# Kernel optimization log

Hardware: AMD Instinct MI355X
Metric: run time of the kernel (lower is better)

## Reference

```python
import jax, jax.numpy as jnp
import numpy as np

NQ, NT, NA = 10000, 50000, 50000
E_GR, E_LT, E_SIM, E_COMP, E_GEN = 50000, 50000, 80000, 100000, 50000
HID, NH, HC, DOT, NL = 512, 4, 128, 256, 2
NEG_SLOPE = 0.2  # PyG GATv2Conv default negative_slope


def _gatv2(x_src, x_dst, src, dst, Wl, bl, Wr, br, att, bias, n_dst):
    # GATv2: x_j = lin_l(x_src), x_i = lin_r(x_dst); e = att . leaky_relu(x_i + x_j)
    xl = (x_src @ Wl + bl).reshape(-1, NH, HC)   # [Ns,H,C]
    xr = (x_dst @ Wr + br).reshape(-1, NH, HC)   # [Nd,H,C]
    m = jax.nn.leaky_relu(xl[src] + xr[dst], NEG_SLOPE)      # [E,H,C]
    logits = jnp.einsum('ehc,hc->eh', m, att)                # [E,H]
    lmax = jax.lax.stop_gradient(jax.ops.segment_max(logits, dst, num_segments=n_dst))
    lmax = jnp.where(jnp.isfinite(lmax), lmax, 0.0)
    ex = jnp.exp(logits - lmax[dst])
    denom = jax.ops.segment_sum(ex, dst, num_segments=n_dst)
    alpha = ex / (denom[dst] + 1e-16)                        # softmax over incoming edges
    out = jax.ops.segment_sum(xl[src] * alpha[:, :, None], dst, num_segments=n_dst)
    return out.reshape(n_dst, NH * HC) + bias


def _layernorm(x, g, b):
    mu = x.mean(-1, keepdims=True)
    var = ((x - mu) ** 2).mean(-1, keepdims=True)
    return (x - mu) / jnp.sqrt(var + 1e-5) * g + b


def _forward(xq, xt, xa, answer_features,
             qp_W, qp_b, tp_W, tp_b, ap_W, ap_b,
             afp_W1, afp_b1, afp_W2, afp_b2,
             conv_Wl, conv_bl, conv_Wr, conv_br, conv_att, conv_bias,
             qh_W, qh_b, qh_g, qh_beta, rh_W, rh_b, rh_g, rh_beta, score_bias,
             ei_gr, ei_lt, ei_sim, ei_comp, ei_gen):
    hq = xq @ qp_W + qp_b
    ht = xt @ tp_W + tp_b
    ha = xa @ ap_W + ap_b
    # add_self_loops=True only for ('query','similar_to','query')
    loops = jnp.arange(NQ, dtype=ei_sim.dtype)
    sim_src = jnp.concatenate([ei_sim[0], loops])
    sim_dst = jnp.concatenate([ei_sim[1], loops])
    for l in range(NL):
        P = lambda r: (conv_Wl[l, r], conv_bl[l, r], conv_Wr[l, r], conv_br[l, r], conv_att[l, r], conv_bias[l, r])
        o_gr = _gatv2(hq, ht, ei_gr[0], ei_gr[1], *P(0), NT)          # query -> think
        o_rgr = _gatv2(ht, hq, ei_gr[1], ei_gr[0], *P(1), NQ)         # think -> query (rev)
        o_lt = _gatv2(ht, ha, ei_lt[0], ei_lt[1], *P(2), NA)          # think -> answer
        o_rlt = _gatv2(ha, ht, ei_lt[1], ei_lt[0], *P(3), NT)         # answer -> think (rev)
        o_sim = _gatv2(hq, hq, sim_src, sim_dst, *P(4), NQ)           # query -> query
        o_cmp = _gatv2(ht, ht, ei_comp[0], ei_comp[1], *P(5), NT)     # think -> think
        # HeteroConv aggr='mean' across relations per destination type, then relu
        hq = jax.nn.relu((o_rgr + o_sim) / 2.0)
        ht = jax.nn.relu((o_gr + o_rlt + o_cmp) / 3.0)
        ha = jax.nn.relu(o_lt)
    q_emb = hq[ei_gen[0]]
    a_emb = ha[ei_gen[1]]
    t_emb = ht[ei_gen[1]]  # faithful to source: think indexed with answer-side index
    af_emb = jax.nn.relu(answer_features @ afp_W1 + afp_b1) @ afp_W2 + afp_b2
    q = _layernorm(q_emb @ qh_W + qh_b, qh_g, qh_beta)
    r = _layernorm(jnp.concatenate([t_emb, a_emb, af_emb], -1) @ rh_W + rh_b, rh_g, rh_beta)
    return (q * r).sum(-1) / jnp.sqrt(jnp.float32(DOT)) + score_bias


def setup_inputs() -> dict:
    ks = jax.random.split(jax.random.key(0), 40)
    n = lambda j, shape, s=0.05: jax.random.normal(ks[j], shape, jnp.float32) * s
    ri = lambda j, shape, hi: jax.random.randint(ks[j], shape, 0, hi, jnp.int32)
    return dict(
        xq=n(0, (NQ, 384), 1.0), xt=n(1, (NT, 384), 1.0), xa=n(2, (NA, 384), 1.0),
        answer_features=n(3, (E_GEN, 6), 1.0),
        qp_W=n(4, (384, HID)), qp_b=n(5, (HID,)),
        tp_W=n(6, (384, HID)), tp_b=n(7, (HID,)),
        ap_W=n(8, (384, HID)), ap_b=n(9, (HID,)),
        afp_W1=n(10, (6, 64)), afp_b1=n(11, (64,)),
        afp_W2=n(12, (64, HID)), afp_b2=n(13, (HID,)),
        conv_Wl=n(14, (NL, 6, HID, HID)), conv_bl=n(15, (NL, 6, HID)),
        conv_Wr=n(16, (NL, 6, HID, HID)), conv_br=n(17, (NL, 6, HID)),
        conv_att=n(18, (NL, 6, NH, HC)), conv_bias=n(19, (NL, 6, HID)),
        qh_W=n(20, (HID, DOT)), qh_b=n(21, (DOT,)),
        qh_g=jnp.ones((DOT,), jnp.float32), qh_beta=jnp.zeros((DOT,), jnp.float32),
        rh_W=n(22, (HID * 3, DOT)), rh_b=n(23, (DOT,)),
        rh_g=jnp.ones((DOT,), jnp.float32), rh_beta=jnp.zeros((DOT,), jnp.float32),
        score_bias=jnp.zeros((1,), jnp.float32),
        ei_gr=jnp.stack([ri(24, (E_GR,), NQ), ri(25, (E_GR,), NT)]),
        ei_lt=jnp.stack([ri(26, (E_LT,), NT), ri(27, (E_LT,), NA)]),
        ei_sim=ri(28, (2, E_SIM), NQ),
        ei_comp=ri(29, (2, E_COMP), NT),
        ei_gen=jnp.stack([ri(30, (E_GEN,), NQ), ri(31, (E_GEN,), NA)]),
    )


def reference(xq, xt, xa, answer_features,
              qp_W, qp_b, tp_W, tp_b, ap_W, ap_b,
              afp_W1, afp_b1, afp_W2, afp_b2,
              conv_Wl, conv_bl, conv_Wr, conv_br, conv_att, conv_bias,
              qh_W, qh_b, qh_g, qh_beta, rh_W, rh_b, rh_g, rh_beta, score_bias,
              ei_gr, ei_lt, ei_sim, ei_comp, ei_gen):
    return _forward(xq, xt, xa, answer_features,
                    qp_W, qp_b, tp_W, tp_b, ap_W, ap_b,
                    afp_W1, afp_b1, afp_W2, afp_b2,
                    conv_Wl, conv_bl, conv_Wr, conv_br, conv_att, conv_bias,
                    qh_W, qh_b, qh_g, qh_beta, rh_W, rh_b, rh_g, rh_beta, score_bias,
                    ei_gr, ei_lt, ei_sim, ei_comp, ei_gen)
```

## Files before the change

kernel.cpp:

```cpp
#include <hip/hip_runtime.h>
#include <cstdio>
#include <type_traits>

#define NQ 10000
#define NT 50000
#define NA 50000
#define E_GR 50000
#define E_LT 50000
#define E_SIM 80000
#define E_COMP 100000
#define E_GEN 50000
#define NEG_SLOPE 0.2f

#define NDTOT 220000
#define ETOT  390000
__device__ __constant__ const int c_degOff[7]  = {0, 50000, 60000, 110000, 120000, 170000, 220000};
__device__ __constant__ const int c_eOff[7]    = {0, 50000, 100000, 150000, 240000, 340000, 390000};
__device__ __constant__ const int c_nb[6]      = {49, 10, 49, 10, 49, 49};
__device__ __constant__ const int c_nbOff[7]   = {0, 49, 59, 108, 118, 167, 216};

typedef unsigned short bf16_t;
typedef unsigned int u32;
typedef __attribute__((ext_vector_type(8))) short short8v;
typedef __attribute__((ext_vector_type(4))) float f32x4;

__device__ __forceinline__ float bf2f(u32 bits) { return __uint_as_float(bits << 16); }
__device__ __forceinline__ u32 f2bf(float f) {
  u32 u = __float_as_uint(f);
  return (u + 0x7FFFu + ((u >> 16) & 1u)) >> 16;
}
__device__ __forceinline__ u32 pack2(float a, float b) { return f2bf(a) | (f2bf(b) << 16); }
__device__ __forceinline__ void unpack8(uint4 u, float* f) {
  f[0] = bf2f(u.x & 0xffffu); f[1] = bf2f(u.x >> 16);
  f[2] = bf2f(u.y & 0xffffu); f[3] = bf2f(u.y >> 16);
  f[4] = bf2f(u.z & 0xffffu); f[5] = bf2f(u.z >> 16);
  f[6] = bf2f(u.w & 0xffffu); f[7] = bf2f(u.w >> 16);
}

__device__ __forceinline__ void gload16(const void* g, void* l) {
  __builtin_amdgcn_global_load_lds(
      (const __attribute__((address_space(1))) void*)g,
      (__attribute__((address_space(3))) void*)l, 16, 0, 0);
}

template <typename CT>
__global__ __launch_bounds__(512, 4) void bgemm(
    const bf16_t* __restrict__ A0, const bf16_t* __restrict__ Bt0,
    const float* __restrict__ bias0, CT* __restrict__ C0,
    const int* __restrict__ ridx0, int N0, const int* __restrict__ Nc0,
    const bf16_t* __restrict__ A1, const bf16_t* __restrict__ Bt1,
    const float* __restrict__ bias1, CT* __restrict__ C1,
    const int* __restrict__ ridx1, int N1, const int* __restrict__ Nc1,
    int K, int M, int accumulate)
{
  __shared__ short lds[3][12288];
  const int z = blockIdx.z;
  const bf16_t* A   = z ? A1 : A0;
  const bf16_t* Bt  = z ? Bt1 : Bt0;
  const float* bias = z ? bias1 : bias0;
  CT* C             = z ? C1 : C0;
  const int* ridx   = z ? ridx1 : ridx0;
  const int* Nc     = z ? Nc1 : Nc0;
  int N             = z ? N1 : N0;
  if (Nc) N = *Nc;

  const int tid = threadIdx.x;
  const int ncol = gridDim.x;
  const int nband = (N + 127) >> 7;
  int lin = blockIdx.y * ncol + blockIdx.x;
  if (lin >= ncol * nband) return;

  int band, col;
  const int full = (nband >> 3) * 8 * ncol;
  if (lin < full) {
    int g = lin >> 3, x = lin & 7;
    band = x + 8 * (g / ncol);
    col  = g % ncol;
  } else {
    int r = lin - full;
    band = (nband & ~7) + r / ncol;
    col  = r % ncol;
  }
  const int bm = band * 128, bn = col * 256;

  const int lane = tid & 63;
  const int w = tid >> 6;
  const int wr = w >> 2, wc = w & 3;
  const int fr = lane & 15, fg = lane >> 4;

  const int kg = (((tid & 3) ^ ((tid >> 3) & 3)) << 3);
  const int rr = tid >> 2;
  int ra = min(bm + rr, N - 1);
  const bf16_t* gA0 = A + (size_t)(ridx ? ridx[ra] : ra) * K + kg;
  const bf16_t* gB0 = Bt + (size_t)(bn + rr) * K + kg;
  const bf16_t* gB1 = Bt + (size_t)(bn + 128 + rr) * K + kg;
  const int wb = w << 9;

  f32x4 acc[4][4];
#pragma unroll
  for (int i = 0; i < 4; ++i)
#pragma unroll
    for (int j = 0; j < 4; ++j) acc[i][j] = (f32x4){0.f, 0.f, 0.f, 0.f};

  auto stage = [&](int buf, int k0) {
    short* base = &lds[buf][0];
    gload16(gA0 + k0, base + wb);
    gload16(gB0 + k0, base + 4096 + wb);
    gload16(gB1 + k0, base + 8192 + wb);
  };

  const int nsteps = K >> 5;
  stage(0, 0);
  const int co = (fg ^ ((fr >> 1) & 3)) << 3;
  for (int s = 0; s < nsteps; ++s) {
    const int cur = s % 3;
    if (s + 1 < nsteps) {
      stage((s + 1) % 3, (s + 1) << 5);
      asm volatile("s_waitcnt vmcnt(3)" ::: "memory");
    } else {
      asm volatile("s_waitcnt vmcnt(0)" ::: "memory");
    }
    __builtin_amdgcn_s_barrier();
    asm volatile("" ::: "memory");
    const short* LA = &lds[cur][0];
    const short* LB = &lds[cur][4096];
    short8v b[4];
#pragma unroll
    for (int j = 0; j < 4; ++j) {
      int R = wc * 64 + j * 16 + fr;
      b[j] = *(const short8v*)&LB[R * 32 + co];
    }
#pragma unroll
    for (int i = 0; i < 4; ++i) {
      int R = wr * 64 + i * 16 + fr;
      short8v a = *(const short8v*)&LA[R * 32 + co];
#pragma unroll
      for (int j = 0; j < 4; ++j)
        acc[i][j] = __builtin_amdgcn_mfma_f32_16x16x32_bf16(b[j], a,
                                                            acc[i][j], 0, 0, 0);
    }
    asm volatile("" ::: "memory");
  }

  float4 bv[4];
#pragma unroll
  for (int j = 0; j < 4; ++j) {
    bv[j] = make_float4(0.f, 0.f, 0.f, 0.f);
    if (!accumulate && bias)
      bv[j] = *(const float4*)(bias + bn + wc * 64 + j * 16 + fg * 4);
  }
#pragma unroll
  for (int i = 0; i < 4; ++i) {
    const int n = bm + wr * 64 + i * 16 + fr;
    if (n >= N) continue;
#pragma unroll
    for (int j = 0; j < 4; ++j) {
      const int m0 = bn + wc * 64 + j * 16 + fg * 4;
      f32x4 v = acc[i][j];
      if constexpr (std::is_same<CT, float>::value) {
        float* p = C + (size_t)n * M + m0;
        if (accumulate) {
          float4 o = *(float4*)p;
          o.x += v[0]; o.y += v[1]; o.z += v[2]; o.w += v[3];
          *(float4*)p = o;
        } else {
          *(float4*)p = make_float4(v[0] + bv[j].x, v[1] + bv[j].y,
                                    v[2] + bv[j].z, v[3] + bv[j].w);
        }
      } else {
        uint2 o;
        o.x = pack2(v[0] + bv[j].x, v[1] + bv[j].y);
        o.y = pack2(v[2] + bv[j].z, v[3] + bv[j].w);
        *(uint2*)(C + (size_t)n * M + m0) = o;
      }
    }
  }
}

__device__ __forceinline__ void wT_tile(
    const float* __restrict__ W, bf16_t* __restrict__ Wt, int K, int M)
{
  __shared__ float sm[32][33];
  int mb = blockIdx.x * 32, kb = blockIdx.y * 32;
  int tx = threadIdx.x & 31, ty = threadIdx.x >> 5;
#pragma unroll
  for (int i = 0; i < 4; ++i)
    sm[ty + i * 8][tx] = W[(size_t)(kb + ty + i * 8) * M + mb + tx];
  __syncthreads();
#pragma unroll
  for (int i = 0; i < 4; ++i)
    Wt[(size_t)(mb + ty + i * 8) * K + kb + tx] = (bf16_t)f2bf(sm[tx][ty + i * 8]);
}

__global__ __launch_bounds__(256) void convert_wT(
    const float* __restrict__ W, bf16_t* __restrict__ Wt, int K, int M)
{
  wT_tile(W + (size_t)blockIdx.z * K * M, Wt + (size_t)blockIdx.z * K * M, K, M);
}
__global__ __launch_bounds__(256) void convert_wT24(
    const float* __restrict__ Wl, bf16_t* __restrict__ wl,
    const float* __restrict__ Wr, bf16_t* __restrict__ wr)
{
  int z = blockIdx.z;
  size_t o = (size_t)(z < 12 ? z : z - 12) * 512 * 512;
  if (z < 12) wT_tile(Wl + o, wl + o, 512, 512);
  else        wT_tile(Wr + o, wr + o, 512, 512);
}
__global__ __launch_bounds__(256) void convert_wT3(
    const float* __restrict__ W0, const float* __restrict__ W1,
    const float* __restrict__ W2, bf16_t* __restrict__ T0,
    bf16_t* __restrict__ T1, bf16_t* __restrict__ T2)
{
  int z = blockIdx.z;
  const float* W = z == 0 ? W0 : z == 1 ? W1 : W2;
  bf16_t* T = z == 0 ? T0 : z == 1 ? T1 : T2;
  wT_tile(W, T, 384, 512);
}
__global__ __launch_bounds__(256) void convert_wT4h(
    const float* __restrict__ qh, const float* __restrict__ rh,
    bf16_t* __restrict__ wqh, bf16_t* __restrict__ wrh)
{
  int z = blockIdx.z;
  if (z == 0) wT_tile(qh, wqh, 512, 256);
  else        wT_tile(rh + (size_t)(z - 1) * 512 * 256,
                      wrh + (size_t)(z - 1) * 256 * 512, 512, 256);
}

#define N4_XQ (NQ * 96)
#define N4_XT (NT * 96)
#define N4_XA (NA * 96)
__global__ __launch_bounds__(256) void cast3(
    const float* __restrict__ xq, const float* __restrict__ xt,
    const float* __restrict__ xa, bf16_t* __restrict__ xqb,
    bf16_t* __restrict__ xtb, bf16_t* __restrict__ xab)
{
  long g = (long)blockIdx.x * 256 + threadIdx.x;
  const float* in; bf16_t* out; long idx;
  if (g < N4_XQ)                { in = xq; out = xqb; idx = g; }
  else if (g < N4_XQ + N4_XT)   { in = xt; out = xtb; idx = g - N4_XQ; }
  else if (g < N4_XQ + N4_XT + N4_XA) { in = xa; out = xab; idx = g - N4_XQ - N4_XT; }
  else return;
  float4 v = ((const float4*)in)[idx];
  uint2 o;
  o.x = pack2(v.x, v.y);
  o.y = pack2(v.z, v.w);
  ((uint2*)out)[idx] = o;
}

__global__ __launch_bounds__(256) void combine_bias6(
    const float* __restrict__ cb, float* __restrict__ bcAll)
{
  int g = blockIdx.x * 256 + threadIdx.x;
  if (g >= 6 * 512) return;
  int row = g >> 9, j = g & 511;
  int l = row / 3, kind = row % 3;
  const float* b = cb + (size_t)l * 6 * 512;
  float v;
  if (kind == 0)      v = (b[0 * 512 + j] + b[3 * 512 + j] + b[5 * 512 + j]) / 3.f;
  else if (kind == 1) v = (b[1 * 512 + j] + b[4 * 512 + j]) * 0.5f;
  else                v = b[2 * 512 + j];
  bcAll[(size_t)row * 512 + j] = v;
}

__device__ __forceinline__ int find_rel(int g, const int* off) {
  int r = 0;
#pragma unroll
  for (int k = 1; k < 6; ++k) r += (g >= off[k]);
  return r;
}

__global__ __launch_bounds__(256) void hist6(
    const int* __restrict__ d0, const int* __restrict__ d1,
    const int* __restrict__ d2, const int* __restrict__ d3,
    const int* __restrict__ d4, const int* __restrict__ d5,
    int* __restrict__ degAll, int* __restrict__ pos)
{
  int g = blockIdx.x * 256 + threadIdx.x;
  if (g >= ETOT) return;
  int r = find_rel(g, c_eOff);
  int le = g - c_eOff[r];
  const int* dp = r == 0 ? d0 : r == 1 ? d1 : r == 2 ? d2 : r == 3 ? d3
                : r == 4 ? d4 : d5;
  pos[g] = atomicAdd(&degAll[c_degOff[r] + dp[le]], 1);
}

template <int PRED>
__global__ __launch_bounds__(256) void scan1_6(
    const int* __restrict__ in, int* __restrict__ out, int* __restrict__ bsum)
{
  __shared__ int sm[256];
  int b = blockIdx.x;
  int r = 0;
#pragma unroll
  for (int k = 1; k < 6; ++k) r += (b >= c_nbOff[k]);
  int lb = b - c_nbOff[r];
  int base0 = c_degOff[r], n = c_degOff[r + 1] - base0;
  int t = threadIdx.x;
  int base = lb * 1024 + t * 4;
  int v[4], sum = 0;
#pragma unroll
  for (int k = 0; k < 4; ++k) {
    int raw = (base + k < n) ? in[base0 + base + k] : 0;
    v[k] = PRED ? (raw >= 2 ? 1 : 0) : raw;
    sum += v[k];
  }
  sm[t] = sum;
  __syncthreads();
  for (int off = 1; off < 256; off <<= 1) {
    int x = (t >= off) ? sm[t - off] : 0;
    __syncthreads();
    sm[t] += x;
    __syncthreads();
  }
  int run = (t > 0) ? sm[t - 1] : 0;
  if (t == 255) bsum[r * 64 + lb] = sm[255];
#pragma unroll
  for (int k = 0; k < 4; ++k) {
    if (base + k < n) out[base0 + base + k] = run;
    run += v[k];
  }
}

__global__ __launch_bounds__(64) void scan2_6(
    int* __restrict__ bsum, int* __restrict__ total)
{
  __shared__ int sm[64];
  int r = blockIdx.x;
  int nb = c_nb[r];
  int t = threadIdx.x;
  int v = (t < nb) ? bsum[r * 64 + t] : 0;
  sm[t] = v;
  __syncthreads();
  for (int off = 1; off < 64; off <<= 1) {
    int x = (t >= off) ? sm[t - off] : 0;
    __syncthreads();
    sm[t] += x;
    __syncthreads();
  }
  if (t < nb) bsum[r * 64 + t] = sm[t] - v;
  if (total && t == nb - 1) total[r] = sm[t];
}

__global__ __launch_bounds__(256) void scan3_6(
    int* __restrict__ out, const int* __restrict__ bsum)
{
  int g = blockIdx.x * 256 + threadIdx.x;
  if (g >= NDTOT) return;
  int r = find_rel(g, c_degOff);
  int ln = g - c_degOff[r];
  out[g] += bsum[r * 64 + (ln >> 10)];
}

__global__ __launch_bounds__(256) void scatter6(
    const int* __restrict__ d0, const int* __restrict__ d1,
    const int* __restrict__ d2, const int* __restrict__ d3,
    const int* __restrict__ d4, const int* __restrict__ d5,
    const int* __restrict__ startAll, const int* __restrict__ pos,
    int* __restrict__ eidxAll)
{
  int g = blockIdx.x * 256 + threadIdx.x;
  if (g >= ETOT) return;
  int r = find_rel(g, c_eOff);
  int le = g - c_eOff[r];
  const int* dp = r == 0 ? d0 : r == 1 ? d1 : r == 2 ? d2 : r == 3 ? d3
                : r == 4 ? d4 : d5;
  eidxAll[c_eOff[r] + startAll[c_degOff[r] + dp[le]] + pos[g]] = le;
}

__global__ __launch_bounds__(256) void compact6(
    const int* __restrict__ degAll, const int* __restrict__ cposAll,
    int* __restrict__ cidxAll)
{
  int g = blockIdx.x * 256 + threadIdx.x;
  if (g >= NDTOT) return;
  if (degAll[g] >= 2) {
    int r = find_rel(g, c_degOff);
    cidxAll[c_degOff[r] + cposAll[g]] = g - c_degOff[r];
  }
}

__global__ __launch_bounds__(256) void gat_fused(
    const bf16_t* __restrict__ xl, const bf16_t* __restrict__ xr,
    const int* __restrict__ srcArr, const int* __restrict__ start,
    const int* __restrict__ deg, const int* __restrict__ eidx,
    const int* __restrict__ cpos, const float* __restrict__ att,
    bf16_t* __restrict__ acc, int Nd, int accumulate,
    const float* __restrict__ bc, float inv_div)
{
  int d = blockIdx.x * 4 + (threadIdx.x >> 6);
  if (d >= Nd) return;
  int lane = threadIdx.x & 63;

  float acc8[8] = {0.f, 0.f, 0.f, 0.f, 0.f, 0.f, 0.f, 0.f};
  int n = deg[d], s0 = start[d];
  if (n == 1) {
    int s = srcArr[eidx[s0]];
    unpack8(*(const uint4*)(xl + (size_t)s * 512 + lane * 8), acc8);
  } else if (n > 1) {
    float xrr[8];
    unpack8(*(const uint4*)(xr + (size_t)cpos[d] * 512 + lane * 8), xrr);
    float at[8];
    *(float4*)(at)     = *(const float4*)(att + lane * 8);
    *(float4*)(at + 4) = *(const float4*)(att + lane * 8 + 4);
    float den = 0.f;
    int sN = srcArr[eidx[s0]];
    for (int i = 0; i < n; ++i) {
      int s = sN;
      if (i + 1 < n) sN = srcArr[eidx[s0 + i + 1]];
      float f[8];
      unpack8(*(const uint4*)(xl + (size_t)s * 512 + lane * 8), f);
      float p = 0.f;
#pragma unroll
      for (int k = 0; k < 8; ++k) {
        float x = f[k] + xrr[k];
        p = fmaf(at[k], x >= 0.f ? x : NEG_SLOPE * x, p);
      }
#pragma unroll
      for (int m = 8; m >= 1; m >>= 1) p += __shfl_xor(p, m);
      float ex = __expf(p);
      den += ex;
#pragma unroll
      for (int k = 0; k < 8; ++k) acc8[k] = fmaf(ex, f[k], acc8[k]);
    }
    float inv = 1.f / (den + 1e-16f);
#pragma unroll
    for (int k = 0; k < 8; ++k) acc8[k] *= inv;
  }

  bf16_t* out = acc + (size_t)d * 512 + lane * 8;
  if (accumulate) {
    float old[8];
    unpack8(*(const uint4*)out, old);
#pragma unroll
    for (int k = 0; k < 8; ++k) acc8[k] += old[k];
  }
  if (bc) {
    float bcv[8];
    *(float4*)(bcv)     = *(const float4*)(bc + lane * 8);
    *(float4*)(bcv + 4) = *(const float4*)(bc + lane * 8 + 4);
#pragma unroll
    for (int k = 0; k < 8; ++k)
      acc8[k] = fmaxf(fmaf(acc8[k], inv_div, bcv[k]), 0.f);
  }
  uint4 s;
  s.x = pack2(acc8[0], acc8[1]); s.y = pack2(acc8[2], acc8[3]);
  s.z = pack2(acc8[4], acc8[5]); s.w = pack2(acc8[6], acc8[7]);
  *(uint4*)out = s;
}

__global__ __launch_bounds__(256) void af_hidden(
    const float* __restrict__ af, const float* __restrict__ W1,
    const float* __restrict__ b1, bf16_t* __restrict__ out, int n)
{
  int t = blockIdx.x * blockDim.x + threadIdx.x;
  if (t >= n * 64) return;
  int i = t >> 6, j = t & 63;
  const float* a = af + (size_t)i * 6;
  float s = b1[j];
#pragma unroll
  for (int k = 0; k < 6; ++k) s = fmaf(a[k], W1[k * 64 + j], s);
  out[t] = (bf16_t)f2bf(fmaxf(s, 0.f));
}

__global__ __launch_bounds__(256) void build_sim(
    const int* __restrict__ ei, int* __restrict__ ss, int* __restrict__ sd)
{
  int t = blockIdx.x * blockDim.x + threadIdx.x;
  if (t >= E_SIM + NQ) return;
  if (t < E_SIM) { ss[t] = ei[t]; sd[t] = ei[E_SIM + t]; }
  else           { ss[t] = t - E_SIM; sd[t] = t - E_SIM; }
}

__global__ __launch_bounds__(256) void head_final(
    const float* __restrict__ qpre, const float* __restrict__ rpre,
    const float* __restrict__ qg, const float* __restrict__ qb,
    const float* __restrict__ rg, const float* __restrict__ rb,
    const float* __restrict__ score_bias, float* __restrict__ out, int E)
{
  int e = blockIdx.x * 4 + (threadIdx.x >> 6);
  if (e >= E) return;
  int lane = threadIdx.x & 63;

  float4 q = *(const float4*)(qpre + (size_t)e * 256 + lane * 4);
  float s = q.x + q.y + q.z + q.w;
#pragma unroll
  for (int m = 32; m >= 1; m >>= 1) s += __shfl_xor(s, m);
  float mu = s * (1.f / 256.f);
  float dq0 = q.x - mu, dq1 = q.y - mu, dq2 = q.z - mu, dq3 = q.w - mu;
  float v = dq0 * dq0 + dq1 * dq1 + dq2 * dq2 + dq3 * dq3;
#pragma unroll
  for (int m = 32; m >= 1; m >>= 1) v += __shfl_xor(v, m);
  float rstd = rsqrtf(v * (1.f / 256.f) + 1e-5f);
  float4 g4 = *(const float4*)(qg + lane * 4);
  float4 b4 = *(const float4*)(qb + lane * 4);
  float qn0 = dq0 * rstd * g4.x + b4.x, qn1 = dq1 * rstd * g4.y + b4.y;
  float qn2 = dq2 * rstd * g4.z + b4.z, qn3 = dq3 * rstd * g4.w + b4.w;

  float4 r = *(const float4*)(rpre + (size_t)e * 256 + lane * 4);
  s = r.x + r.y + r.z + r.w;
#pragma unroll
  for (int m = 32; m >= 1; m >>= 1) s += __shfl_xor(s, m);
  mu = s * (1.f / 256.f);
  float dr0 = r.x - mu, dr1 = r.y - mu, dr2 = r.z - mu, dr3 = r.w - mu;
  v = dr0 * dr0 + dr1 * dr1 + dr2 * dr2 + dr3 * dr3;
#pragma unroll
  for (int m = 32; m >= 1; m >>= 1) v += __shfl_xor(v, m);
  rstd = rsqrtf(v * (1.f / 256.f) + 1e-5f);
  g4 = *(const float4*)(rg + lane * 4);
  b4 = *(const float4*)(rb + lane * 4);
  float rn0 = dr0 * rstd * g4.x + b4.x, rn1 = dr1 * rstd * g4.y + b4.y;
  float rn2 = dr2 * rstd * g4.z + b4.z, rn3 = dr3 * rstd * g4.w + b4.w;

  float d = qn0 * rn0 + qn1 * rn1 + qn2 * rn2 + qn3 * rn3;
#pragma unroll
  for (int m = 32; m >= 1; m >>= 1) d += __shfl_xor(d, m);
  if (lane == 0) out[e] = d * 0.0625f + score_bias[0];
}

extern "C" void kernel_launch(void* const* d_in, const int* in_sizes, int n_in,
                              void* d_out, int out_size, void* d_ws, size_t ws_size,
                              hipStream_t stream) {
  (void)in_sizes; (void)n_in; (void)out_size;
  const float* xq      = (const float*)d_in[0];
  const float* xt      = (const float*)d_in[1];
  const float* xa      = (const float*)d_in[2];
  const float* af      = (const float*)d_in[3];
  const float* qp_W    = (const float*)d_in[4];
  const float* qp_b    = (const float*)d_in[5];
  const float* tp_W    = (const float*)d_in[6];
  const float* tp_b    = (const float*)d_in[7];
  const float* ap_W    = (const float*)d_in[8];
  const float* ap_b    = (const float*)d_in[9];
  const float* afp_W1  = (const float*)d_in[10];
  const float* afp_b1  = (const float*)d_in[11];
  const float* afp_W2  = (const float*)d_in[12];
  const float* afp_b2  = (const float*)d_in[13];
  const float* conv_Wl = (const float*)d_in[14];
  const float* conv_bl = (const float*)d_in[15];
  const float* conv_Wr = (const float*)d_in[16];
  const float* conv_br = (const float*)d_in[17];
  const float* conv_att  = (const float*)d_in[18];
  const float* conv_bias = (const float*)d_in[19];
  const float* qh_W    = (const float*)d_in[20];
  const float* qh_b    = (const float*)d_in[21];
  const float* qh_g    = (const float*)d_in[22];
  const float* qh_beta = (const float*)d_in[23];
  const float* rh_W    = (const float*)d_in[24];
  const float* rh_b    = (const float*)d_in[25];
  const float* rh_g    = (const float*)d_in[26];
  const float* rh_beta = (const float*)d_in[27];
  const float* score_b = (const float*)d_in[28];
  const int* ei_gr   = (const int*)d_in[29];
  const int* ei_lt   = (const int*)d_in[30];
  const int* ei_sim  = (const int*)d_in[31];
  const int* ei_comp = (const int*)d_in[32];
  const int* ei_gen  = (const int*)d_in[33];

  char* base = (char*)d_ws;
  size_t off = 0;
  auto alloc = [&](size_t bytes) {
    void* p = base + off;
    off = (off + bytes + 255) & ~(size_t)255;
    return p;
  };
  bf16_t* hq   = (bf16_t*)alloc((size_t)NQ * 512 * 2);
  bf16_t* ht   = (bf16_t*)alloc((size_t)NT * 512 * 2);
  bf16_t* ha   = (bf16_t*)alloc((size_t)NA * 512 * 2);
  bf16_t* acct = (bf16_t*)alloc((size_t)NT * 512 * 2);
  bf16_t* accq = (bf16_t*)alloc((size_t)NQ * 512 * 2);
  bf16_t* xlb  = (bf16_t*)alloc((size_t)50000 * 512 * 2);
  bf16_t* xrb  = (bf16_t*)alloc((size_t)50000 * 512 * 2);
  int* simsrc  = (int*)alloc((size_t)(E_SIM + NQ) * 4);
  int* simdst  = (int*)alloc((size_t)(E_SIM + NQ) * 4);

  bf16_t* wqp  = (bf16_t*)alloc((size_t)512 * 384 * 2);
  bf16_t* wtp  = (bf16_t*)alloc((size_t)512 * 384 * 2);
  bf16_t* wap  = (bf16_t*)alloc((size_t)512 * 384 * 2);
  bf16_t* wl   = (bf16_t*)alloc((size_t)12 * 512 * 512 * 2);
  bf16_t* wr   = (bf16_t*)alloc((size_t)12 * 512 * 512 * 2);
  bf16_t* wafp2 = (bf16_t*)alloc((size_t)512 * 64 * 2);
  bf16_t* wqh  = (bf16_t*)alloc((size_t)256 * 512 * 2);
  bf16_t* wrh0 = (bf16_t*)alloc((size_t)256 * 512 * 2);
  bf16_t* wrh1 = (bf16_t*)alloc((size_t)256 * 512 * 2);
  bf16_t* wrh2 = (bf16_t*)alloc((size_t)256 * 512 * 2);
  float* bcAll = (float*)alloc(6 * 512 * 4);

  int* degAll   = (int*)alloc((size_t)NDTOT * 4);
  int* startAll = (int*)alloc((size_t)NDTOT * 4);
  int* cposAll  = (int*)alloc((size_t)NDTOT * 4);
  int* cidxAll  = (int*)alloc((size_t)NDTOT * 4);
  int* eidxAll  = (int*)alloc((size_t)ETOT * 4);
  int* posb     = (int*)alloc((size_t)ETOT * 4);
  int* bsum     = (int*)alloc(6 * 64 * 4);
  int* bsum2    = (int*)alloc(6 * 64 * 4);
  int* ccount   = (int*)alloc(6 * 4);
  if (off > ws_size) {
    fprintf(stderr, "kernel_launch: ws too small, need %zu have %zu\n", off, ws_size);
    return;
  }

  const int degOff[6] = {0, 50000, 60000, 110000, 120000, 170000};
  const int eOff[6]   = {0, 50000, 100000, 150000, 240000, 340000};

  convert_wT24<<<dim3(16, 16, 24), 256, 0, stream>>>(conv_Wl, wl, conv_Wr, wr);
  convert_wT3<<<dim3(16, 12, 3), 256, 0, stream>>>(qp_W, tp_W, ap_W, wqp, wtp, wap);
  convert_wT4h<<<dim3(8, 16, 4), 256, 0, stream>>>(qh_W, rh_W, wqh, wrh0);
  convert_wT<<<dim3(16, 2, 1), 256, 0, stream>>>(afp_W2, wafp2, 64, 512);
  combine_bias6<<<(6 * 512 + 255) / 256, 256, 0, stream>>>(conv_bias, bcAll);

  build_sim<<<(E_SIM + NQ + 255) / 256, 256, 0, stream>>>(ei_sim, simsrc, simdst);
  const int* dsts[6] = {ei_gr + E_GR, ei_gr, ei_lt, simdst,
                        ei_comp + E_COMP, ei_lt + E_LT};
  hipMemsetAsync(degAll, 0, (size_t)NDTOT * 4, stream);
  hist6<<<(ETOT + 255) / 256, 256, 0, stream>>>(dsts[0], dsts[1], dsts[2],
      dsts[3], dsts[4], dsts[5], degAll, posb);
  scan1_6<0><<<216, 256, 0, stream>>>(degAll, startAll, bsum);
  scan1_6<1><<<216, 256, 0, stream>>>(degAll, cposAll, bsum2);
  scan2_6<<<6, 64, 0, stream>>>(bsum, nullptr);
  scan2_6<<<6, 64, 0, stream>>>(bsum2, ccount);
  scan3_6<<<(NDTOT + 255) / 256, 256, 0, stream>>>(startAll, bsum);
  scan3_6<<<(NDTOT + 255) / 256, 256, 0, stream>>>(cposAll, bsum2);
  scatter6<<<(ETOT + 255) / 256, 256, 0, stream>>>(dsts[0], dsts[1], dsts[2],
      dsts[3], dsts[4], dsts[5], startAll, posb, eidxAll);
  compact6<<<(NDTOT + 255) / 256, 256, 0, stream>>>(degAll, cposAll, cidxAll);

  auto gemm1 = [&](const bf16_t* A, const bf16_t* Bt, const float* bias, bf16_t* C,
                   int N_, int K_, int M_, const int* ridx = nullptr) {
    dim3 g(M_ / 256, (N_ + 127) / 128, 1);
    bgemm<bf16_t><<<g, 512, 0, stream>>>(A, Bt, bias, C, ridx, N_, nullptr,
                                         A, Bt, bias, C, ridx, N_, nullptr,
                                         K_, M_, 0);
  };
  auto gemmf1 = [&](const bf16_t* A, const bf16_t* Bt, const float* bias, float* C,
                    int N_, int K_, int M_, int acc_, const int* ridx = nullptr) {
    dim3 g(M_ / 256, (N_ + 127) / 128, 1);
    bgemm<float><<<g, 512, 0, stream>>>(A, Bt, bias, C, ridx, N_, nullptr,
                                        A, Bt, bias, C, ridx, N_, nullptr,
                                        K_, M_, acc_);
  };
  auto gemm2 = [&](const bf16_t* A0, const bf16_t* B0, const float* b0, bf16_t* C0, int N0_,
                   const bf16_t* A1, const bf16_t* B1, const float* b1, bf16_t* C1, int N1_,
                   int K_, int M_) {
    int nb0 = (N0_ + 127) / 128, nb1 = (N1_ + 127) / 128;
    dim3 g(M_ / 256, nb0 > nb1 ? nb0 : nb1, 2);
    bgemm<bf16_t><<<g, 512, 0, stream>>>(A0, B0, b0, C0, nullptr, N0_, nullptr,
                                         A1, B1, b1, C1, nullptr, N1_, nullptr,
                                         K_, M_, 0);
  };
  auto gemm2c = [&](const bf16_t* A0, const bf16_t* B0, const float* b0, bf16_t* C0, int N0_,
                    const bf16_t* A1, const bf16_t* B1, const float* b1, bf16_t* C1,
                    const int* cidx, int N1max, const int* Ncnt) {
    int nb0 = (N0_ + 127) / 128, nb1 = (N1max + 127) / 128;
    dim3 g(2, nb0 > nb1 ? nb0 : nb1, 2);
    bgemm<bf16_t><<<g, 512, 0, stream>>>(A0, B0, b0, C0, nullptr, N0_, nullptr,
                                         A1, B1, b1, C1, cidx, N1max, Ncnt,
                                         512, 512, 0);
  };
  auto gemmf2 = [&](const bf16_t* A0, const bf16_t* B0, const float* b0, float* C0,
                    const int* r0, int N0_,
                    const bf16_t* A1, const bf16_t* B1, const float* b1, float* C1,
                    const int* r1, int N1_, int K_, int M_) {
    int nb0 = (N0_ + 127) / 128, nb1 = (N1_ + 127) / 128;
    dim3 g(M_ / 256, nb0 > nb1 ? nb0 : nb1, 2);
    bgemm<float><<<g, 512, 0, stream>>>(A0, B0, b0, C0, r0, N0_, nullptr,
                                        A1, B1, b1, C1, r1, N1_, nullptr,
                                        K_, M_, 0);
  };

  cast3<<<((long)(N4_XQ + N4_XT + N4_XA) + 255) / 256, 256, 0, stream>>>(
      xq, xt, xa, accq, xlb, xrb);
  gemm1(accq, wqp, qp_b, hq, NQ, 384, 512);
  gemm2(xlb, wtp, tp_b, ht, NT, xrb, wap, ap_b, ha, NA, 384, 512);

  const int* srcs[6] = {ei_gr, ei_gr + E_GR, ei_lt + E_LT, simsrc,
                        ei_comp, ei_lt};
  const int NdArr[6] = {NT, NQ, NT, NQ, NT, NA};
  bf16_t *hq_i = hq, *ht_i = ht, *hq_o = accq, *ht_o = acct;
  for (int l = 0; l < 2; ++l) {
    const float* bc_t = bcAll + (size_t)(l * 3 + 0) * 512;
    const float* bc_q = bcAll + (size_t)(l * 3 + 1) * 512;
    const float* bc_a = bcAll + (size_t)(l * 3 + 2) * 512;

    struct Rel { const bf16_t* xs; const bf16_t* xd; int Ns, po; bf16_t* acc;
                 int accum; const float* bc; float inv; };
    Rel rels[6] = {
      {hq_i, ht_i, NQ, 0, ht_o, 0, nullptr, 0.f},
      {ht_i, hq_i, NT, 1, hq_o, 0, nullptr, 0.f},
      {ha,   ht_i, NA, 3, ht_o, 1, nullptr, 0.f},
      {hq_i, hq_i, NQ, 4, hq_o, 1, bc_q, 0.5f},
      {ht_i, ht_i, NT, 5, ht_o, 1, bc_t, 1.f / 3.f},
      {ht_i, ha,   NT, 2, ha,   0, bc_a, 1.f},
    };
    for (int r = 0; r < 6; ++r) {
      const Rel& R = rels[r];
      int Nd_ = NdArr[r];
      size_t po = (size_t)l * 6 + R.po;
      gemm2c(R.xs, wl + po * 512 * 512, conv_bl + po * 512, xlb, R.Ns,
             R.xd, wr + po * 512 * 512, conv_br + po * 512, xrb,
             cidxAll + degOff[r], Nd_, ccount + r);
      int gb = (Nd_ + 3) / 4;
      gat_fused<<<gb, 256, 0, stream>>>(xlb, xrb, srcs[r],
                                        startAll + degOff[r], degAll + degOff[r],
                                        eidxAll + eOff[r], cposAll + degOff[r],
                                        conv_att + po * 512,
                                        R.acc, Nd_, R.accum, R.bc, R.inv);
    }
    bf16_t* t;
    t = hq_i; hq_i = hq_o; hq_o = t;
    t = ht_i; ht_i = ht_o; ht_o = t;
  }

  float* qpre = (float*)acct;
  float* rpre = (float*)xrb;
  bf16_t* afh = accq;
  const int* gsrc = ei_gen;
  const int* gdst = ei_gen + E_GEN;

  gemmf2(hq_i, wqh, qh_b, qpre, gsrc, E_GEN,
         ht_i, wrh0, rh_b, rpre, gdst, E_GEN, 512, 256);
  gemmf1(ha, wrh1, nullptr, rpre, E_GEN, 512, 256, 1, gdst);
  af_hidden<<<(E_GEN * 64 + 255) / 256, 256, 0, stream>>>(af, afp_W1, afp_b1,
                                                          afh, E_GEN);
  gemm1(afh, wafp2, afp_b2, xlb, E_GEN, 64, 512);
  gemmf1(xlb, wrh2, nullptr, rpre, E_GEN, 512, 256, 1);
  head_final<<<(E_GEN + 3) / 4, 256, 0, stream>>>(
      qpre, rpre, qh_g, qh_beta, rh_g, rh_beta, score_b, (float*)d_out, E_GEN);
}
```

Measured before the change: 1.269 ms.

## Compact source-node lin_l GEMM to only nodes that appear as edge sources

Builds a per-relation source-degree histogram, scans it, and compacts the list of source nodes with at least one outgoing edge. The lin_l GEMM for each relation then computes rows only for those used sources, and edges are remapped to compacted row indices so the attention kernel reads the compacted xl buffer. This skips projection work for unreferenced source nodes, which with random edges is a notable fraction for the 50k-node types. In exchange it adds extra atomics, scans and scatter kernels to the preprocessing.

```diff
diff --git a/kernel.cpp b/kernel.cpp
--- a/kernel.cpp
+++ b/kernel.cpp
@@ -13,11 +13,15 @@
 #define NEG_SLOPE 0.2f
 
 #define NDTOT 220000
+#define NSTOT 220000
 #define ETOT  390000
 __device__ __constant__ const int c_degOff[7]  = {0, 50000, 60000, 110000, 120000, 170000, 220000};
+__device__ __constant__ const int c_sOff[7]    = {0, 10000, 60000, 110000, 120000, 170000, 220000};
 __device__ __constant__ const int c_eOff[7]    = {0, 50000, 100000, 150000, 240000, 340000, 390000};
 __device__ __constant__ const int c_nb[6]      = {49, 10, 49, 10, 49, 49};
 __device__ __constant__ const int c_nbOff[7]   = {0, 49, 59, 108, 118, 167, 216};
+__device__ __constant__ const int c_snb[6]     = {10, 49, 49, 10, 49, 49};
+__device__ __constant__ const int c_snbOff[7]  = {0, 10, 59, 108, 118, 167, 216};
 
 typedef unsigned short bf16_t;
 typedef unsigned int u32;
@@ -262,7 +266,7 @@
   bcAll[(size_t)row * 512 + j] = v;
 }
 
-__device__ __forceinline__ int find_rel(int g, const int* off) {
+__device__ __forceinline__ int find_rel6(int g, const int* off) {
   int r = 0;
 #pragma unroll
   for (int k = 1; k < 6; ++k) r += (g >= off[k]);
@@ -273,35 +277,43 @@
     const int* __restrict__ d0, const int* __restrict__ d1,
     const int* __restrict__ d2, const int* __restrict__ d3,
     const int* __restrict__ d4, const int* __restrict__ d5,
-    int* __restrict__ degAll, int* __restrict__ pos)
+    const int* __restrict__ s0p, const int* __restrict__ s1p,
+    const int* __restrict__ s2p, const int* __restrict__ s3p,
+    const int* __restrict__ s4p, const int* __restrict__ s5p,
+    int* __restrict__ degAll, int* __restrict__ sdegAll, int* __restrict__ pos)
 {
   int g = blockIdx.x * 256 + threadIdx.x;
   if (g >= ETOT) return;
-  int r = find_rel(g, c_eOff);
+  int r = find_rel6(g, c_eOff);
   int le = g - c_eOff[r];
   const int* dp = r == 0 ? d0 : r == 1 ? d1 : r == 2 ? d2 : r == 3 ? d3
                 : r == 4 ? d4 : d5;
+  const int* sp = r == 0 ? s0p : r == 1 ? s1p : r == 2 ? s2p : r == 3 ? s3p
+                : r == 4 ? s4p : s5p;
   pos[g] = atomicAdd(&degAll[c_degOff[r] + dp[le]], 1);
-}
-
-template <int PRED>
+  atomicAdd(&sdegAll[c_sOff[r] + sp[le]], 1);
+}
+
+template <int PRED, int SRC>
 __global__ __launch_bounds__(256) void scan1_6(
     const int* __restrict__ in, int* __restrict__ out, int* __restrict__ bsum)
 {
   __shared__ int sm[256];
   int b = blockIdx.x;
+  const int* nbOff = SRC ? c_snbOff : c_nbOff;
+  const int* dOff  = SRC ? c_sOff : c_degOff;
   int r = 0;
 #pragma unroll
-  for (int k = 1; k < 6; ++k) r += (b >= c_nbOff[k]);
-  int lb = b - c_nbOff[r];
-  int base0 = c_degOff[r], n = c_degOff[r + 1] - base0;
+  for (int k = 1; k < 6; ++k) r += (b >= nbOff[k]);
+  int lb = b - nbOff[r];
+  int base0 = dOff[r], n = dOff[r + 1] - base0;
   int t = threadIdx.x;
   int base = lb * 1024 + t * 4;
   int v[4], sum = 0;
 #pragma unroll
   for (int k = 0; k < 4; ++k) {
     int raw = (base + k < n) ? in[base0 + base + k] : 0;
-    v[k] = PRED ? (raw >= 2 ? 1 : 0) : raw;
+    v[k] = PRED == 0 ? raw : PRED == 1 ? (raw >= 2 ? 1 : 0) : (raw >= 1 ? 1 : 0);
     sum += v[k];
   }
   sm[t] = sum;
@@ -321,12 +333,13 @@
   }
 }
 
+template <int SRC>
 __global__ __launch_bounds__(64) void scan2_6(
     int* __restrict__ bsum, int* __restrict__ total)
 {
   __shared__ int sm[64];
   int r = blockIdx.x;
-  int nb = c_nb[r];
+  int nb = SRC ? c_snb[r] : c_nb[r];
   int t = threadIdx.x;
   int v = (t < nb) ? bsum[r * 64 + t] : 0;
   sm[t] = v;
@@ -341,13 +354,15 @@
   if (total && t == nb - 1) total[r] = sm[t];
 }
 
+template <int SRC>
 __global__ __launch_bounds__(256) void scan3_6(
     int* __restrict__ out, const int* __restrict__ bsum)
 {
   int g = blockIdx.x * 256 + threadIdx.x;
-  if (g >= NDTOT) return;
-  int r = find_rel(g, c_degOff);
-  int ln = g - c_degOff[r];
+  if (g >= (SRC ? NSTOT : NDTOT)) return;
+  const int* dOff = SRC ? c_sOff : c_degOff;
+  int r = find_rel6(g, dOff);
+  int ln = g - dOff[r];
   out[g] += bsum[r * 64 + (ln >> 10)];
 }
 
@@ -355,33 +370,42 @@
     const int* __restrict__ d0, const int* __restrict__ d1,
     const int* __restrict__ d2, const int* __restrict__ d3,
     const int* __restrict__ d4, const int* __restrict__ d5,
+    const int* __restrict__ s0p, const int* __restrict__ s1p,
+    const int* __restrict__ s2p, const int* __restrict__ s3p,
+    const int* __restrict__ s4p, const int* __restrict__ s5p,
     const int* __restrict__ startAll, const int* __restrict__ pos,
-    int* __restrict__ eidxAll)
+    const int* __restrict__ sposAll,
+    int* __restrict__ eidxAll, int* __restrict__ srcCAll)
 {
   int g = blockIdx.x * 256 + threadIdx.x;
   if (g >= ETOT) return;
-  int r = find_rel(g, c_eOff);
+  int r = find_rel6(g, c_eOff);
   int le = g - c_eOff[r];
   const int* dp = r == 0 ? d0 : r == 1 ? d1 : r == 2 ? d2 : r == 3 ? d3
                 : r == 4 ? d4 : d5;
+  const int* sp = r == 0 ? s0p : r == 1 ? s1p : r == 2 ? s2p : r == 3 ? s3p
+                : r == 4 ? s4p : s5p;
   eidxAll[c_eOff[r] + startAll[c_degOff[r] + dp[le]] + pos[g]] = le;
-}
-
+  srcCAll[g] = sposAll[c_sOff[r] + sp[le]];
+}
+
+template <int SRC, int THR>
 __global__ __launch_bounds__(256) void compact6(
-    const int* __restrict__ degAll, const int* __restrict__ cposAll,
-    int* __restrict__ cidxAll)
+    const int* __restrict__ degA, const int* __restrict__ cposA,
+    int* __restrict__ cidxA)
 {
   int g = blockIdx.x * 256 + threadIdx.x;
-  if (g >= NDTOT) return;
-  if (degAll[g] >= 2) {
-    int r = find_rel(g, c_degOff);
-    cidxAll[c_degOff[r] + cposAll[g]] = g - c_degOff[r];
+  if (g >= (SRC ? NSTOT : NDTOT)) return;
+  if (degA[g] >= THR) {
+    const int* dOff = SRC ? c_sOff : c_degOff;
+    int r = find_rel6(g, dOff);
+    cidxA[dOff[r] + cposA[g]] = g - dOff[r];
   }
 }
 
 __global__ __launch_bounds__(256) void gat_fused(
     const bf16_t* __restrict__ xl, const bf16_t* __restrict__ xr,
-    const int* __restrict__ srcArr, const int* __restrict__ start,
+    const int* __restrict__ srcC, const int* __restrict__ start,
     const int* __restrict__ deg, const int* __restrict__ eidx,
     const int* __restrict__ cpos, const float* __restrict__ att,
     bf16_t* __restrict__ acc, int Nd, int accumulate,
@@ -394,7 +418,7 @@
   float acc8[8] = {0.f, 0.f, 0.f, 0.f, 0.f, 0.f, 0.f, 0.f};
   int n = deg[d], s0 = start[d];
   if (n == 1) {
-    int s = srcArr[eidx[s0]];
+    int s = srcC[eidx[s0]];
     unpack8(*(const uint4*)(xl + (size_t)s * 512 + lane * 8), acc8);
   } else if (n > 1) {
     float xrr[8];
@@ -403,10 +427,10 @@
     *(float4*)(at)     = *(const float4*)(att + lane * 8);
     *(float4*)(at + 4) = *(const float4*)(att + lane * 8 + 4);
     float den = 0.f;
-    int sN = srcArr[eidx[s0]];
+    int sN = srcC[eidx[s0]];
     for (int i = 0; i < n; ++i) {
       int s = sN;
-      if (i + 1 < n) sN = srcArr[eidx[s0 + i + 1]];
+      if (i + 1 < n) sN = srcC[eidx[s0 + i + 1]];
       float f[8];
       unpack8(*(const uint4*)(xl + (size_t)s * 512 + lane * 8), f);
       float p = 0.f;
@@ -589,17 +613,24 @@
   int* startAll = (int*)alloc((size_t)NDTOT * 4);
   int* cposAll  = (int*)alloc((size_t)NDTOT * 4);
   int* cidxAll  = (int*)alloc((size_t)NDTOT * 4);
+  int* sdegAll  = (int*)alloc((size_t)NSTOT * 4);
+  int* sposAll  = (int*)alloc((size_t)NSTOT * 4);
+  int* sidxAll  = (int*)alloc((size_t)NSTOT * 4);
   int* eidxAll  = (int*)alloc((size_t)ETOT * 4);
+  int* srcCAll  = (int*)alloc((size_t)ETOT * 4);
   int* posb     = (int*)alloc((size_t)ETOT * 4);
   int* bsum     = (int*)alloc(6 * 64 * 4);
   int* bsum2    = (int*)alloc(6 * 64 * 4);
+  int* sbsum    = (int*)alloc(6 * 64 * 4);
   int* ccount   = (int*)alloc(6 * 4);
+  int* scount   = (int*)alloc(6 * 4);
   if (off > ws_size) {
     fprintf(stderr, "kernel_launch: ws too small, need %zu have %zu\n", off, ws_size);
     return;
   }
 
   const int degOff[6] = {0, 50000, 60000, 110000, 120000, 170000};
+  const int sOff[6]   = {0, 10000, 60000, 110000, 120000, 170000};
   const int eOff[6]   = {0, 50000, 100000, 150000, 240000, 340000};
 
   convert_wT24<<<dim3(16, 16, 24), 256, 0, stream>>>(conv_Wl, wl, conv_Wr, wr);
@@ -609,20 +640,31 @@
   combine_bias6<<<(6 * 512 + 255) / 256, 256, 0, stream>>>(conv_bias, bcAll);
 
   build_sim<<<(E_SIM + NQ + 255) / 256, 256, 0, stream>>>(ei_sim, simsrc, simdst);
-  const int* dsts[6] = {ei_gr + E_GR, ei_gr, ei_lt, simdst,
-                        ei_comp + E_COMP, ei_lt + E_LT};
+  const int* dsts[6]  = {ei_gr + E_GR, ei_gr, ei_lt, simdst,
+                         ei_comp + E_COMP, ei_lt + E_LT};
+  const int* srcsA[6] = {ei_gr, ei_gr + E_GR, ei_lt + E_LT, simsrc,
+                         ei_comp, ei_lt};
   hipMemsetAsync(degAll, 0, (size_t)NDTOT * 4, stream);
-  hist6<<<(ETOT + 255) / 256, 256, 0, stream>>>(dsts[0], dsts[1], dsts[2],
-      dsts[3], dsts[4], dsts[5], degAll, posb);
-  scan1_6<0><<<216, 256, 0, stream>>>(degAll, startAll, bsum);
-  scan1_6<1><<<216, 256, 0, stream>>>(degAll, cposAll, bsum2);
-  scan2_6<<<6, 64, 0, stream>>>(bsum, nullptr);
-  scan2_6<<<6, 64, 0, stream>>>(bsum2, ccount);
-  scan3_6<<<(NDTOT + 255) / 256, 256, 0, stream>>>(startAll, bsum);
-  scan3_6<<<(NDTOT + 255) / 256, 256, 0, stream>>>(cposAll, bsum2);
-  scatter6<<<(ETOT + 255) / 256, 256, 0, stream>>>(dsts[0], dsts[1], dsts[2],
-      dsts[3], dsts[4], dsts[5], startAll, posb, eidxAll);
-  compact6<<<(NDTOT + 255) / 256, 256, 0, stream>>>(degAll, cposAll, cidxAll);
+  hipMemsetAsync(sdegAll, 0, (size_t)NSTOT * 4, stream);
+  hist6<<<(ETOT + 255) / 256, 256, 0, stream>>>(
+      dsts[0], dsts[1], dsts[2], dsts[3], dsts[4], dsts[5],
+      srcsA[0], srcsA[1], srcsA[2], srcsA[3], srcsA[4], srcsA[5],
+      degAll, sdegAll, posb);
+  scan1_6<0, 0><<<216, 256, 0, stream>>>(degAll, startAll, bsum);
+  scan1_6<1, 0><<<216, 256, 0, stream>>>(degAll, cposAll, bsum2);
+  scan1_6<2, 1><<<216, 256, 0, stream>>>(sdegAll, sposAll, sbsum);
+  scan2_6<0><<<6, 64, 0, stream>>>(bsum, nullptr);
+  scan2_6<0><<<6, 64, 0, stream>>>(bsum2, ccount);
+  scan2_6<1><<<6, 64, 0, stream>>>(sbsum, scount);
+  scan3_6<0><<<(NDTOT + 255) / 256, 256, 0, stream>>>(startAll, bsum);
+  scan3_6<0><<<(NDTOT + 255) / 256, 256, 0, stream>>>(cposAll, bsum2);
+  scan3_6<1><<<(NSTOT + 255) / 256, 256, 0, stream>>>(sposAll, sbsum);
+  scatter6<<<(ETOT + 255) / 256, 256, 0, stream>>>(
+      dsts[0], dsts[1], dsts[2], dsts[3], dsts[4], dsts[5],
+      srcsA[0], srcsA[1], srcsA[2], srcsA[3], srcsA[4], srcsA[5],
+      startAll, posb, sposAll, eidxAll, srcCAll);
+  compact6<0, 2><<<(NDTOT + 255) / 256, 256, 0, stream>>>(degAll, cposAll, cidxAll);
+  compact6<1, 1><<<(NSTOT + 255) / 256, 256, 0, stream>>>(sdegAll, sposAll, sidxAll);
 
   auto gemm1 = [&](const bf16_t* A, const bf16_t* Bt, const float* bias, bf16_t* C,
                    int N_, int K_, int M_, const int* ridx = nullptr) {
@@ -647,12 +689,13 @@
                                          A1, B1, b1, C1, nullptr, N1_, nullptr,
                                          K_, M_, 0);
   };
-  auto gemm2c = [&](const bf16_t* A0, const bf16_t* B0, const float* b0, bf16_t* C0, int N0_,
-                    const bf16_t* A1, const bf16_t* B1, const float* b1, bf16_t* C1,
-                    const int* cidx, int N1max, const int* Ncnt) {
-    int nb0 = (N0_ + 127) / 128, nb1 = (N1max + 127) / 128;
+  auto gemm2cc = [&](const bf16_t* A0, const bf16_t* B0, const float* b0, bf16_t* C0,
+                     const int* sidx, int N0max, const int* Ns_,
+                     const bf16_t* A1, const bf16_t* B1, const float* b1, bf16_t* C1,
+                     const int* cidx, int N1max, const int* Ncnt) {
+    int nb0 = (N0max + 127) / 128, nb1 = (N1max + 127) / 128;
     dim3 g(2, nb0 > nb1 ? nb0 : nb1, 2);
-    bgemm<bf16_t><<<g, 512, 0, stream>>>(A0, B0, b0, C0, nullptr, N0_, nullptr,
+    bgemm<bf16_t><<<g, 512, 0, stream>>>(A0, B0, b0, C0, sidx, N0max, Ns_,
                                          A1, B1, b1, C1, cidx, N1max, Ncnt,
                                          512, 512, 0);
   };
@@ -672,34 +715,34 @@
   gemm1(accq, wqp, qp_b, hq, NQ, 384, 512);
   gemm2(xlb, wtp, tp_b, ht, NT, xrb, wap, ap_b, ha, NA, 384, 512);
 
-  const int* srcs[6] = {ei_gr, ei_gr + E_GR, ei_lt + E_LT, simsrc,
-                        ei_comp, ei_lt};
   const int NdArr[6] = {NT, NQ, NT, NQ, NT, NA};
+  const int NsArr[6] = {NQ, NT, NA, NQ, NT, NT};
   bf16_t *hq_i = hq, *ht_i = ht, *hq_o = accq, *ht_o = acct;
   for (int l = 0; l < 2; ++l) {
     const float* bc_t = bcAll + (size_t)(l * 3 + 0) * 512;
     const float* bc_q = bcAll + (size_t)(l * 3 + 1) * 512;
     const float* bc_a = bcAll + (size_t)(l * 3 + 2) * 512;
 
-    struct Rel { const bf16_t* xs; const bf16_t* xd; int Ns, po; bf16_t* acc;
+    struct Rel { const bf16_t* xs; const bf16_t* xd; int po; bf16_t* acc;
                  int accum; const float* bc; float inv; };
     Rel rels[6] = {
-      {hq_i, ht_i, NQ, 0, ht_o, 0, nullptr, 0.f},
-      {ht_i, hq_i, NT, 1, hq_o, 0, nullptr, 0.f},
-      {ha,   ht_i, NA, 3, ht_o, 1, nullptr, 0.f},
-      {hq_i, hq_i, NQ, 4, hq_o, 1, bc_q, 0.5f},
-      {ht_i, ht_i, NT, 5, ht_o, 1, bc_t, 1.f / 3.f},
-      {ht_i, ha,   NT, 2, ha,   0, bc_a, 1.f},
+      {hq_i, ht_i, 0, ht_o, 0, nullptr, 0.f},
+      {ht_i, hq_i, 1, hq_o, 0, nullptr, 0.f},
+      {ha,   ht_i, 3, ht_o, 1, nullptr, 0.f},
+      {hq_i, hq_i, 4, hq_o, 1, bc_q, 0.5f},
+      {ht_i, ht_i, 5, ht_o, 1, bc_t, 1.f / 3.f},
+      {ht_i, ha,   2, ha,   0, bc_a, 1.f},
     };
     for (int r = 0; r < 6; ++r) {
       const Rel& R = rels[r];
       int Nd_ = NdArr[r];
       size_t po = (size_t)l * 6 + R.po;
-      gemm2c(R.xs, wl + po * 512 * 512, conv_bl + po * 512, xlb, R.Ns,
-             R.xd, wr + po * 512 * 512, conv_br + po * 512, xrb,
-             cidxAll + degOff[r], Nd_, ccount + r);
+      gemm2cc(R.xs, wl + po * 512 * 512, conv_bl + po * 512, xlb,
+              sidxAll + sOff[r], NsArr[r], scount + r,
+              R.xd, wr + po * 512 * 512, conv_br + po * 512, xrb,
+              cidxAll + degOff[r], Nd_, ccount + r);
       int gb = (Nd_ + 3) / 4;
-      gat_fused<<<gb, 256, 0, stream>>>(xlb, xrb, srcs[r],
+      gat_fused<<<gb, 256, 0, stream>>>(xlb, xrb, srcCAll + eOff[r],
                                         startAll + degOff[r], degAll + degOff[r],
                                         eidxAll + eOff[r], cposAll + degOff[r],
                                         conv_att + po * 512,
```

Result: no change. 1.251 ms (-1.4%).
